# Performance work log

Measured on AMD Instinct MI355X. Metric: run time of the kernel, lower is better.

Reference implementation:

```python
import jax, jax.numpy as jnp
import numpy as np

DOF = 7
HID = 30
L_DIM = DOF * (DOF + 1) // 2  # 28
BATCH = 262144


def _linear_params(key, d_in, d_out, scale=0.3):
    k1, k2 = jax.random.split(key)
    W = jax.random.normal(k1, (d_out, d_in), dtype=jnp.float32) * scale / np.sqrt(d_in)
    b = jax.random.normal(k2, (d_out,), dtype=jnp.float32) * 0.01
    return W, b


def setup_inputs() -> dict:
    key = jax.random.key(0)
    ks = jax.random.split(key, 11)
    x = jax.random.normal(ks[0], (BATCH, 3 * DOF), dtype=jnp.float32)
    ld_w1, ld_b1 = _linear_params(ks[1], DOF, HID)
    ld_w2, ld_b2 = _linear_params(ks[2], HID, DOF)
    lo_w1, lo_b1 = _linear_params(ks[3], DOF, HID)
    lo_w2, lo_b2 = _linear_params(ks[4], HID, L_DIM - DOF)
    g_w1, g_b1 = _linear_params(ks[5], DOF, HID)
    g_w2, g_b2 = _linear_params(ks[6], HID, DOF)
    m_w1, m_b1 = _linear_params(ks[7], L_DIM + DOF, HID)
    m_w2, m_b2 = _linear_params(ks[8], HID, DOF)
    c_w1, c_b1 = _linear_params(ks[9], L_DIM * DOF + DOF, HID)
    c_w2, c_b2 = _linear_params(ks[10], HID, DOF)
    return dict(x=x,
                ld_w1=ld_w1, ld_b1=ld_b1, ld_w2=ld_w2, ld_b2=ld_b2,
                lo_w1=lo_w1, lo_b1=lo_b1, lo_w2=lo_w2, lo_b2=lo_b2,
                g_w1=g_w1, g_b1=g_b1, g_w2=g_w2, g_b2=g_b2,
                m_w1=m_w1, m_b1=m_b1, m_w2=m_w2, m_b2=m_b2,
                c_w1=c_w1, c_b1=c_b1, c_w2=c_w2, c_b2=c_b2)


def _sin_net_with_jac(q, W1, b1, W2, b2):
    # 2-layer SinNet: out = W2 @ sin(W1 q + b1) + b2, plus analytic batched Jacobian.
    pre = q @ W1.T + b1                 # [B, H]
    out = jnp.sin(pre) @ W2.T + b2      # [B, O]
    # d out_o / d q_d = sum_h W2[o,h] * cos(pre)[b,h] * W1[h,d]
    jac = jnp.einsum('oh,bh,hd->bod', W2, jnp.cos(pre), W1)  # [B, O, DOF]
    return out, jac


def _sigmoid_net(z, W1, b1, W2, b2):
    return jax.nn.sigmoid(z @ W1.T + b1) @ W2.T + b2


def reference(x,
              ld_w1, ld_b1, ld_w2, ld_b2,
              lo_w1, lo_b1, lo_w2, lo_b2,
              g_w1, g_b1, g_w2, g_b2,
              m_w1, m_b1, m_w2, m_b2,
              c_w1, c_b1, c_w2, c_b2):
    q = x[:, :DOF]
    qDot = x[:, DOF:2 * DOF]
    qDDot = x[:, 2 * DOF:3 * DOF]

    h_ld, jac_ld = _sin_net_with_jac(q, ld_w1, ld_b1, ld_w2, ld_b2)  # [B,DOF], [B,DOF,DOF]
    h_lo, jac_lo = _sin_net_with_jac(q, lo_w1, lo_b1, lo_w2, lo_b2)  # [B,L-D], [B,L-D,DOF]

    h_l = jnp.concatenate([h_ld, h_lo], axis=1)          # [B, L_DIM]
    m = _sigmoid_net(jnp.concatenate([h_l, qDDot], axis=1), m_w1, m_b1, m_w2, m_b2)

    # dl[:, i*DOF:(i+1)*DOF] = d h_l[:, i] / d q  -> flatten [B, L_DIM, DOF]
    dl = jnp.concatenate([jac_ld, jac_lo], axis=1).reshape(x.shape[0], L_DIM * DOF)
    c = _sigmoid_net(jnp.concatenate([dl, qDot], axis=1), c_w1, c_b1, c_w2, c_b2)

    g = jnp.sin(q @ g_w1.T + g_b1) @ g_w2.T + g_b2
    return m + c + g
```

## Files before the change

### kernel.cpp

```cpp
#include <hip/hip_runtime.h>


#define NT 256

typedef short bf16x8 __attribute__((ext_vector_type(8)));
typedef float f32x4  __attribute__((ext_vector_type(4)));

__device__ inline unsigned short f2b(float f) {
    union { float f; unsigned u; } v; v.f = f;
    return (unsigned short)((v.u + 0x7FFF + ((v.u >> 16) & 1)) >> 16);
}

constexpr int PW_LD = 0;
constexpr int PW_LO = 1024;
constexpr int PW_G  = 2048;
constexpr int PB_MZ = 3072;
constexpr int PB_CZ = 6144;
constexpr int PB_O  = 9216;
constexpr int NPACK = 10752;

__global__ void precompute_kernel(
    const float* __restrict__ ld_w1, const float* __restrict__ ld_b1,
    const float* __restrict__ ld_w2, const float* __restrict__ ld_b2,
    const float* __restrict__ lo_w1, const float* __restrict__ lo_b1,
    const float* __restrict__ lo_w2, const float* __restrict__ lo_b2,
    const float* __restrict__ g_w1,  const float* __restrict__ g_b1,
    const float* __restrict__ g_w2,  const float* __restrict__ g_b2,
    const float* __restrict__ m_w1,  const float* __restrict__ m_b1,
    const float* __restrict__ m_w2,  const float* __restrict__ m_b2,
    const float* __restrict__ c_w1,  const float* __restrict__ c_b1,
    const float* __restrict__ c_w2,  const float* __restrict__ c_b2,
    float* __restrict__ ws)
{
    int i = blockIdx.x * blockDim.x + threadIdx.x;
    if (i < 16) { ws[i] = (i < 7) ? (m_b2[i] + c_b2[i] + g_b2[i]) : 0.f; return; }
    int r = i - 16;
    if (r >= NPACK) return;
    unsigned short* wp = (unsigned short*)ws + 32;
    float val = 0.f;
    if (r < 3072) {
        int tb = r / 1024, rr = r % 1024;
        int nc = rr >> 9, n = (rr >> 5) & 15, k = rr & 31, h = nc * 16 + n;
        const float* W1 = (tb == 0) ? ld_w1 : (tb == 1) ? lo_w1 : g_w1;
        const float* B1 = (tb == 0) ? ld_b1 : (tb == 1) ? lo_b1 : g_b1;
        if (h < 30) { if (k < 7) val = W1[h*7 + k]; else if (k == 7) val = B1[h]; }
    } else if (r < 6144) {
        int rr = r - 3072; int kc = rr >> 10; rr &= 1023;
        int nc = rr >> 9, n = (rr >> 5) & 15, k = rr & 31, j = nc * 16 + n;
        if (j < 30) {
            if (kc == 0) {
                if (k < 30) { float a = 0.f;
                    for (int o = 0; o < 7; ++o) a += m_w1[j*35 + o] * ld_w2[o*30 + k];
                    val = a; }
            } else if (kc == 1) {
                if (k < 30) { float a = 0.f;
                    for (int o = 0; o < 21; ++o) a += m_w1[j*35 + 7 + o] * lo_w2[o*30 + k];
                    val = a; }
            } else {
                if (k < 7) val = m_w1[j*35 + 28 + k];
                else if (k == 7) { float a = m_b1[j];
                    for (int o = 0; o < 7;  ++o) a += m_w1[j*35 + o]     * ld_b2[o];
                    for (int o = 0; o < 21; ++o) a += m_w1[j*35 + 7 + o] * lo_b2[o];
                    val = a; }
            }
        }
    } else if (r < 9216) {
        int rr = r - 6144; int kc = rr >> 10; rr &= 1023;
        int nc = rr >> 9, n = (rr >> 5) & 15, k = rr & 31, j = nc * 16 + n;
        if (j < 30) {
            if (kc == 0) {
                if (k < 30) { float a = 0.f;
                    for (int o = 0; o < 7; ++o) { float t = 0.f;
                        for (int d = 0; d < 7; ++d) t += c_w1[j*203 + o*7 + d] * ld_w1[k*7 + d];
                        a += ld_w2[o*30 + k] * t; }
                    val = a; }
            } else if (kc == 1) {
                if (k < 30) { float a = 0.f;
                    for (int o = 0; o < 21; ++o) { float t = 0.f;
                        for (int d = 0; d < 7; ++d) t += c_w1[j*203 + (7+o)*7 + d] * lo_w1[k*7 + d];
                        a += lo_w2[o*30 + k] * t; }
                    val = a; }
            } else {
                if (k < 7) val = c_w1[j*203 + 196 + k];
                else if (k == 7) val = c_b1[j];
            }
        }
    } else {
        int rr = r - 9216; int kc = rr >> 9, n = (rr >> 5) & 15, k = rr & 31;
        if (n < 7 && k < 30)
            val = ((kc == 0) ? m_w2 : (kc == 1) ? c_w2 : g_w2)[n*30 + k];
    }
    wp[r] = f2b(val);
}

#define MFMA(a, b, c) __builtin_amdgcn_mfma_f32_16x16x32_bf16((a), (b), (c), 0, 0, 0)

__global__ __launch_bounds__(NT, 3) void delan_main(
    const float* __restrict__ x, const float* __restrict__ ws, float* __restrict__ out)
{
    __shared__ __align__(16) unsigned short L[4 * 3968];
    const int lane = threadIdx.x & 63, wid = threadIdx.x >> 6;
    const int n15 = lane & 15, quad = lane >> 4;
    unsigned short* Ls = L + wid * 3968;
    unsigned short* Lc = Ls + 1152;
    unsigned short* Lg = Ls + 2304;

    const unsigned short* wp = (const unsigned short*)ws + 32;
    const int fo = n15 * 32 + quad * 8;

    bf16x8 bw_ld[2], bw_lo[2], bw_g[2], bm[3][2], bc[3][2], bo[3];
#pragma unroll
    for (int c = 0; c < 2; ++c) {
        bw_ld[c] = *(const bf16x8*)(wp + PW_LD + c*512 + fo);
        bw_lo[c] = *(const bf16x8*)(wp + PW_LO + c*512 + fo);
        bw_g[c]  = *(const bf16x8*)(wp + PW_G  + c*512 + fo);
#pragma unroll
        for (int kc = 0; kc < 3; ++kc) {
            bm[kc][c] = *(const bf16x8*)(wp + PB_MZ + kc*1024 + c*512 + fo);
            bc[kc][c] = *(const bf16x8*)(wp + PB_CZ + kc*1024 + c*512 + fo);
        }
    }
#pragma unroll
    for (int kc = 0; kc < 3; ++kc)
        bo[kc] = *(const bf16x8*)(wp + PB_O + kc*512 + fo);
    const float bout = ws[n15];

    const f32x4 zero4 = {0.f, 0.f, 0.f, 0.f};

    for (int t = 0; t < 4; ++t) {
        const int eb = blockIdx.x * 256 + wid * 64 + t * 16;

        float xq[21];
#pragma unroll
        for (int d = 0; d < 21; ++d) xq[d] = 0.f;
        if (quad == 0) {
            const float* xp = x + (size_t)(eb + n15) * 21;
#pragma unroll
            for (int d = 0; d < 21; ++d) xq[d] = xp[d];
        }

        bf16x8 a0;
#pragma unroll
        for (int d = 0; d < 7; ++d) a0[d] = (short)f2b(xq[d]);
        a0[7] = (quad == 0) ? (short)0x3F80 : (short)0;

        f32x4 pld[2], plo[2], pg[2];
#pragma unroll
        for (int c = 0; c < 2; ++c) {
            pld[c] = MFMA(a0, bw_ld[c], zero4);
            plo[c] = MFMA(a0, bw_lo[c], zero4);
            pg[c]  = MFMA(a0, bw_g[c],  zero4);
        }

#pragma unroll
        for (int c = 0; c < 2; ++c) {
            const int h = c * 16 + n15;
#pragma unroll
            for (int rg = 0; rg < 4; ++rg) {
                const int m = quad * 4 + rg;
                float p1 = pld[c][rg];
                Ls[m*72 + h]      = f2b(__sinf(p1));
                Lc[m*72 + h]      = f2b(__cosf(p1));
                float p2 = plo[c][rg];
                Ls[m*72 + 32 + h] = f2b(__sinf(p2));
                Lc[m*72 + 32 + h] = f2b(__cosf(p2));
                Lg[m*104 + 64 + h] = f2b(__sinf(pg[c][rg]));
            }
        }

        bf16x8 as0 = *(const bf16x8*)(Ls + n15*72 + quad*8);
        bf16x8 as1 = *(const bf16x8*)(Ls + n15*72 + 32 + quad*8);
        bf16x8 ac0 = *(const bf16x8*)(Lc + n15*72 + quad*8);
        bf16x8 ac1 = *(const bf16x8*)(Lc + n15*72 + 32 + quad*8);
        bf16x8 add_, aqd_;
#pragma unroll
        for (int d = 0; d < 7; ++d) { add_[d] = (short)f2b(xq[14 + d]); aqd_[d] = (short)f2b(xq[7 + d]); }
        add_[7] = a0[7]; aqd_[7] = a0[7];

        f32x4 mz[2], cz[2];
#pragma unroll
        for (int c = 0; c < 2; ++c) {
            f32x4 m_ = MFMA(as0, bm[0][c], zero4);
            m_ = MFMA(as1, bm[1][c], m_);
            mz[c] = MFMA(add_, bm[2][c], m_);
            f32x4 c_ = MFMA(ac0, bc[0][c], zero4);
            c_ = MFMA(ac1, bc[1][c], c_);
            cz[c] = MFMA(aqd_, bc[2][c], c_);
        }

#pragma unroll
        for (int c = 0; c < 2; ++c) {
            const int j = c * 16 + n15;
#pragma unroll
            for (int rg = 0; rg < 4; ++rg) {
                const int m = quad * 4 + rg;
                Lg[m*104 + j]      = f2b(__builtin_amdgcn_rcpf(1.f + __expf(-mz[c][rg])));
                Lg[m*104 + 32 + j] = f2b(__builtin_amdgcn_rcpf(1.f + __expf(-cz[c][rg])));
            }
        }

        bf16x8 ag0 = *(const bf16x8*)(Lg + n15*104 + quad*8);
        bf16x8 ag1 = *(const bf16x8*)(Lg + n15*104 + 32 + quad*8);
        bf16x8 ag2 = *(const bf16x8*)(Lg + n15*104 + 64 + quad*8);
        f32x4 o = MFMA(ag0, bo[0], zero4);
        o = MFMA(ag1, bo[1], o);
        o = MFMA(ag2, bo[2], o);

        if (n15 < 7) {
            float* op = out + (size_t)(eb + quad * 4) * 7 + n15;
            op[0]  = o[0] + bout;
            op[7]  = o[1] + bout;
            op[14] = o[2] + bout;
            op[21] = o[3] + bout;
        }
    }
}

extern "C" void kernel_launch(void* const* d_in, const int* in_sizes, int n_in,
                              void* d_out, int out_size, void* d_ws, size_t ws_size,
                              hipStream_t stream)
{
    const float* x = (const float*)d_in[0];
    float* ws = (float*)d_ws;

    precompute_kernel<<<(16 + NPACK + 255) / 256, 256, 0, stream>>>(
        (const float*)d_in[1],  (const float*)d_in[2],
        (const float*)d_in[3],  (const float*)d_in[4],
        (const float*)d_in[5],  (const float*)d_in[6],
        (const float*)d_in[7],  (const float*)d_in[8],
        (const float*)d_in[9],  (const float*)d_in[10],
        (const float*)d_in[11], (const float*)d_in[12],
        (const float*)d_in[13], (const float*)d_in[14],
        (const float*)d_in[15], (const float*)d_in[16],
        (const float*)d_in[17], (const float*)d_in[18],
        (const float*)d_in[19], (const float*)d_in[20],
        ws);

    const int batch = out_size / 7;
    const int nblk  = batch / NT;
    delan_main<<<nblk, NT, 0, stream>>>(x, ws, (float*)d_out);
}
```

Measured before the change: 133.9 us.

## Stage input rows as packed bf16 in LDS with all threads loading

All 256 threads now load their input row at kernel start, convert it to bf16 and pack it into shared memory with a bias 1.0 in each 8-element group. The per-tile loop then reads the MFMA A-operands straight from LDS instead of 16 lanes per wave loading and converting 21 floats every tile. The aim is to spread global loads across every lane and issue them once, cutting per-tile load latency and conversion work. The cost is extra LDS, a block barrier, and reliance on the packed weights being zero for K positions past 8, since the other quads now read neighbouring data rather than zeros.

Measured after the change: 133.0 us. No clear change (-0.7%).

```diff
diff --git a/kernel.cpp b/kernel.cpp
--- a/kernel.cpp
+++ b/kernel.cpp
@@ -9,6 +9,9 @@
 __device__ inline unsigned short f2b(float f) {
     union { float f; unsigned u; } v; v.f = f;
     return (unsigned short)((v.u + 0x7FFF + ((v.u >> 16) & 1)) >> 16);
+}
+__device__ inline unsigned pk2(float lo, float hi) {
+    return (unsigned)f2b(lo) | ((unsigned)f2b(hi) << 16);
 }
 
 constexpr int PW_LD = 0;
@@ -98,10 +101,33 @@
 __global__ __launch_bounds__(NT, 3) void delan_main(
     const float* __restrict__ x, const float* __restrict__ ws, float* __restrict__ out)
 {
-    __shared__ __align__(16) unsigned short L[4 * 3968];
-    const int lane = threadIdx.x & 63, wid = threadIdx.x >> 6;
+    __shared__ __align__(16) unsigned short xs2[NT * 24 + 32];
+    __shared__ __align__(16) unsigned short Lbuf[4 * 3968];
+
+    const int tid = threadIdx.x;
+    const int lane = tid & 63, wid = tid >> 6;
     const int n15 = lane & 15, quad = lane >> 4;
-    unsigned short* Ls = L + wid * 3968;
+
+    {
+        const float* xp = x + (size_t)(blockIdx.x * NT + tid) * 21;
+        float v[21];
+#pragma unroll
+        for (int d = 0; d < 21; ++d) v[d] = xp[d];
+        int4* dst = (int4*)(xs2 + tid * 24);
+#pragma unroll
+        for (int g = 0; g < 3; ++g) {
+            int4 u;
+            u.x = (int)pk2(v[g*7 + 0], v[g*7 + 1]);
+            u.y = (int)pk2(v[g*7 + 2], v[g*7 + 3]);
+            u.z = (int)pk2(v[g*7 + 4], v[g*7 + 5]);
+            u.w = (int)pk2(v[g*7 + 6], 1.0f);
+            dst[g] = u;
+        }
+    }
+    if (tid < 16) ((unsigned*)(xs2 + NT * 24))[tid] = 0;
+    __syncthreads();
+
+    unsigned short* Ls = Lbuf + wid * 3968;
     unsigned short* Lc = Ls + 1152;
     unsigned short* Lg = Ls + 2304;
 
@@ -127,22 +153,14 @@
 
     const f32x4 zero4 = {0.f, 0.f, 0.f, 0.f};
 
+#pragma unroll 1
     for (int t = 0; t < 4; ++t) {
-        const int eb = blockIdx.x * 256 + wid * 64 + t * 16;
-
-        float xq[21];
-#pragma unroll
-        for (int d = 0; d < 21; ++d) xq[d] = 0.f;
-        if (quad == 0) {
-            const float* xp = x + (size_t)(eb + n15) * 21;
-#pragma unroll
-            for (int d = 0; d < 21; ++d) xq[d] = xp[d];
-        }
-
-        bf16x8 a0;
-#pragma unroll
-        for (int d = 0; d < 7; ++d) a0[d] = (short)f2b(xq[d]);
-        a0[7] = (quad == 0) ? (short)0x3F80 : (short)0;
+        const int elb = wid * 64 + t * 16;
+        const unsigned short* ep = xs2 + (elb + n15) * 24;
+
+        bf16x8 a0  = *(const bf16x8*)(ep + quad * 8);
+        bf16x8 aqd = *(const bf16x8*)(ep + 8 + quad * 8);
+        bf16x8 add = *(const bf16x8*)(ep + 16 + quad * 8);
 
         f32x4 pld[2], plo[2], pg[2];
 #pragma unroll
@@ -159,11 +177,11 @@
             for (int rg = 0; rg < 4; ++rg) {
                 const int m = quad * 4 + rg;
                 float p1 = pld[c][rg];
-                Ls[m*72 + h]      = f2b(__sinf(p1));
-                Lc[m*72 + h]      = f2b(__cosf(p1));
+                Ls[m*72 + h]       = f2b(__sinf(p1));
+                Lc[m*72 + h]       = f2b(__cosf(p1));
                 float p2 = plo[c][rg];
-                Ls[m*72 + 32 + h] = f2b(__sinf(p2));
-                Lc[m*72 + 32 + h] = f2b(__cosf(p2));
+                Ls[m*72 + 32 + h]  = f2b(__sinf(p2));
+                Lc[m*72 + 32 + h]  = f2b(__cosf(p2));
                 Lg[m*104 + 64 + h] = f2b(__sinf(pg[c][rg]));
             }
         }
@@ -172,20 +190,16 @@
         bf16x8 as1 = *(const bf16x8*)(Ls + n15*72 + 32 + quad*8);
         bf16x8 ac0 = *(const bf16x8*)(Lc + n15*72 + quad*8);
         bf16x8 ac1 = *(const bf16x8*)(Lc + n15*72 + 32 + quad*8);
-        bf16x8 add_, aqd_;
-#pragma unroll
-        for (int d = 0; d < 7; ++d) { add_[d] = (short)f2b(xq[14 + d]); aqd_[d] = (short)f2b(xq[7 + d]); }
-        add_[7] = a0[7]; aqd_[7] = a0[7];
 
         f32x4 mz[2], cz[2];
 #pragma unroll
         for (int c = 0; c < 2; ++c) {
             f32x4 m_ = MFMA(as0, bm[0][c], zero4);
             m_ = MFMA(as1, bm[1][c], m_);
-            mz[c] = MFMA(add_, bm[2][c], m_);
+            mz[c] = MFMA(add, bm[2][c], m_);
             f32x4 c_ = MFMA(ac0, bc[0][c], zero4);
             c_ = MFMA(ac1, bc[1][c], c_);
-            cz[c] = MFMA(aqd_, bc[2][c], c_);
+            cz[c] = MFMA(aqd, bc[2][c], c_);
         }
 
 #pragma unroll
@@ -207,6 +221,7 @@
         o = MFMA(ag2, bo[2], o);
 
         if (n15 < 7) {
+            const int eb = blockIdx.x * NT + elb;
             float* op = out + (size_t)(eb + quad * 4) * 7 + n15;
             op[0]  = o[0] + bout;
             op[7]  = o[1] + bout;
```
